# Kernel tuning notes

Hardware: AMD Instinct MI355X
Metric: run time of the kernel (lower is better)

Reference implementation:

```python
import jax, jax.numpy as jnp
import numpy as np

NUM_GROUPS = 32
EPS = 1e-5


def group_norm(x, w, b):
    # x: [B,C,H,W], 32 groups
    B, C, H, W = x.shape
    xg = x.reshape(B, NUM_GROUPS, C // NUM_GROUPS, H, W)
    mean = xg.mean(axis=(2, 3, 4), keepdims=True)
    var = xg.var(axis=(2, 3, 4), keepdims=True)
    xn = ((xg - mean) * jax.lax.rsqrt(var + EPS)).reshape(B, C, H, W)
    return xn * w[None, :, None, None] + b[None, :, None, None]


def conv1x1(x, w, b):
    # x: [B,C,H,W], w: [O,C], b: [O]
    return jnp.einsum('bchw,oc->bohw', x, w) + b[None, :, None, None]


def setup_inputs() -> dict:
    key = jax.random.key(0)
    ks = jax.random.split(key, 7)
    B, C, H, W = 16, 512, 32, 32
    x = jax.random.normal(ks[0], (B, C, H, W), dtype=jnp.float32)
    gn_w = jnp.ones((C,), dtype=jnp.float32)
    gn_b = jnp.zeros((C,), dtype=jnp.float32)
    s = 1.0 / np.sqrt(C)
    qkv_w = jax.random.normal(ks[1], (3 * C, C), dtype=jnp.float32) * s
    qkv_b = jnp.zeros((3 * C,), dtype=jnp.float32)
    proj_w = jax.random.normal(ks[2], (C, C), dtype=jnp.float32) * s
    proj_b = jnp.zeros((C,), dtype=jnp.float32)
    return {"x": x, "gn_w": gn_w, "gn_b": gn_b, "qkv_w": qkv_w,
            "qkv_b": qkv_b, "proj_w": proj_w, "proj_b": proj_b}


def reference(x, gn_w, gn_b, qkv_w, qkv_b, proj_w, proj_b):
    B, C, H, W = x.shape
    qkv = conv1x1(group_norm(x, gn_w, gn_b), qkv_w, qkv_b)
    q, k, v = jnp.split(qkv, 3, axis=1)
    scale = (C // 8) ** (-0.5)
    # attn: [B, h, w, H, W]
    attn = jnp.einsum('bchw,bcHW->bhwHW', q * scale, k)
    # NOTE: faithful to original torch code: softmax over the LAST axis only
    attn = jax.nn.softmax(attn, axis=-1)
    out = jnp.einsum('bhwHW,bcHW->bchw', attn, v)
    return x + conv1x1(out, proj_w, proj_b)
```

## Files before the change

kernel.cpp:

```cpp
#include <hip/hip_runtime.h>
#include <hip/hip_bf16.h>

#define B_    16
#define C_    512
#define S_    1024
#define NGRP  32
#define CPG   16

typedef __attribute__((ext_vector_type(8))) short  short8;
typedef __attribute__((ext_vector_type(4))) short  short4v;
typedef __attribute__((ext_vector_type(4))) float  floatx4;

__device__ __forceinline__ unsigned short f2bf(float f) {
    __hip_bfloat16 h = __float2bfloat16(f);
    unsigned short u;
    __builtin_memcpy(&u, &h, 2);
    return u;
}

__global__ __launch_bounds__(256)
void prep_kernel(const float* __restrict__ qkv_w, const float* __restrict__ proj_w,
                 const float* __restrict__ qkv_b,
                 unsigned short* __restrict__ bufX,
                 unsigned short* __restrict__ bufY,
                 float* __restrict__ bqWk, float* __restrict__ biasvp)
{
    int blk = blockIdx.x;
    int tid = threadIdx.x;
    if (blk < 192) {
        __shared__ float T[64][65];
        int mat = blk >> 6, tile = blk & 63;
        int r0 = (tile >> 3) * 64, c0 = (tile & 7) * 64;
        const float* src; unsigned short* dst;
        if (mat == 0)      { src = qkv_w + 512 * 512;  dst = bufX; }
        else if (mat == 1) { src = qkv_w;              dst = bufY; }
        else               { src = qkv_w + 1024 * 512; dst = bufY + 262144; }
#pragma unroll
        for (int rr = 0; rr < 4; ++rr) {
            int sr = rr * 16 + (tid >> 4);
            int sc = (tid & 15) * 4;
            float4 v = *(const float4*)(src + (size_t)(c0 + sr) * 512 + r0 + sc);
            T[sc][sr] = v.x; T[sc + 1][sr] = v.y; T[sc + 2][sr] = v.z; T[sc + 3][sr] = v.w;
        }
        __syncthreads();
#pragma unroll
        for (int rr = 0; rr < 4; ++rr) {
            int dr = rr * 16 + (tid >> 4);
            int dc = (tid & 15) * 4;
            short4v o;
            o[0] = (short)f2bf(T[dr][dc]);     o[1] = (short)f2bf(T[dr][dc + 1]);
            o[2] = (short)f2bf(T[dr][dc + 2]); o[3] = (short)f2bf(T[dr][dc + 3]);
            *(short4v*)(dst + (size_t)(r0 + dr) * 512 + c0 + dc) = o;
        }
    } else if (blk < 256) {
        unsigned short* wp = bufX + 262144;
#pragma unroll
        for (int t = 0; t < 4; ++t) {
            int i = (blk - 192) * 4096 + t * 1024 + tid * 4;
            float4 v = *(const float4*)(proj_w + i);
            short4v o;
            o[0] = (short)f2bf(v.x); o[1] = (short)f2bf(v.y);
            o[2] = (short)f2bf(v.z); o[3] = (short)f2bf(v.w);
            *(short4v*)(wp + i) = o;
        }
    } else if (blk < 264) {
        int sub = blk - 256;
        int j = (sub & 1) * 256 + tid;
        int o0 = (sub >> 1) * 128;
        float acc = 0.f;
#pragma unroll 8
        for (int oo = 0; oo < 128; ++oo) {
            int o = o0 + oo;
            acc += qkv_b[o] * qkv_w[(size_t)(512 + o) * 512 + j];
        }
        atomicAdd(&bqWk[j], acc);
    } else {
        int wv = tid >> 6, lane = tid & 63;
        int c = (blk - 264) * 4 + wv;
        float s = 0.f;
#pragma unroll
        for (int t = 0; t < 8; ++t)
            s += proj_w[(size_t)c * 512 + t * 64 + lane] * qkv_b[1024 + t * 64 + lane];
        for (int off = 32; off > 0; off >>= 1) s += __shfl_down(s, off);
        if (lane == 0) biasvp[c] = s;
    }
}

__global__ __launch_bounds__(256)
void gn_plus_w(const float* __restrict__ x, const float* __restrict__ gnw,
               const float* __restrict__ gnb, __hip_bfloat16* __restrict__ xnT,
               const unsigned short* __restrict__ bufX,
               const unsigned short* __restrict__ bufY,
               unsigned short* __restrict__ bufZ)
{
    __shared__ __align__(16) char smem[32832];
    int blk = blockIdx.x;
    int tid = threadIdx.x;

    if (blk < 512) {
        int b = blk >> 5, g = blk & 31;
        const float4* xp = (const float4*)(x + (size_t)blk * (CPG * S_));
        float4 vv[16];
        float s = 0.f, ss = 0.f;
#pragma unroll
        for (int r = 0; r < 16; ++r) {
            float4 v = xp[r * 256 + tid];
            vv[r] = v;
            s  += v.x + v.y + v.z + v.w;
            ss += v.x*v.x + v.y*v.y + v.z*v.z + v.w*v.w;
        }
        for (int off = 32; off > 0; off >>= 1) {
            s  += __shfl_down(s, off);
            ss += __shfl_down(ss, off);
        }
        float* red = (float*)(smem + 32768);
        float* msh = (float*)(smem + 32800);
        int wid = tid >> 6, lane = tid & 63;
        if (lane == 0) { red[wid] = s; red[4 + wid] = ss; }
        __syncthreads();
        if (tid == 0) {
            float a = 0.f, c = 0.f;
            for (int i = 0; i < 4; ++i) { a += red[i]; c += red[4 + i]; }
            float mean = a / (float)(CPG * S_);
            float var  = c / (float)(CPG * S_) - mean * mean;
            msh[0] = mean;
            msh[1] = rsqrtf(var + 1e-5f);
        }
        __syncthreads();
        float mean = msh[0], inv = msh[1];

        float sc[16], sh[16];
#pragma unroll
        for (int c = 0; c < 16; ++c) {
            float wc = gnw[g * 16 + c];
            sc[c] = inv * wc;
            sh[c] = gnb[g * 16 + c] - mean * inv * wc;
        }
#pragma unroll
        for (int kk = 0; kk < 4; ++kk) {
            unsigned short outp[16];
#pragma unroll
            for (int c = 0; c < 16; ++c) {
                float v = (kk == 0) ? vv[c].x : (kk == 1) ? vv[c].y : (kk == 2) ? vv[c].z : vv[c].w;
                outp[c] = f2bf(v * sc[c] + sh[c]);
            }
            int srow = 4 * tid + kk;
            unsigned short* dst = (unsigned short*)xnT + ((size_t)(b * S_ + srow) * C_ + g * 16);
            *(short8*)dst       = *(short8*)outp;
            *(short8*)(dst + 8) = *(short8*)(outp + 8);
        }
    } else {
        unsigned short* As = (unsigned short*)smem;
        unsigned short* Bs = (unsigned short*)(smem + 16384);
        int id = blk - 512;
        int bx = id & 3, by = (id >> 2) & 3, bz = id >> 4;
        const unsigned short* Ab = bufX + (size_t)bz * 262144;
        const unsigned short* Bb = bufY + (size_t)bz * 262144;
        __hip_bfloat16* Y = (__hip_bfloat16*)bufZ + (size_t)bz * 262144;
        const int wave = tid >> 6, lane = tid & 63;
        const int m0 = by * 128, n0 = bx * 128;
        const int wr = wave >> 1, wc = wave & 1, lr = lane & 15, kq = lane >> 4;
        const int row0 = tid >> 2, kc0 = (tid & 3) << 3;

        floatx4 acc[4][4] = {};
        for (int k0 = 0; k0 < 512; k0 += 64) {
            __syncthreads();
#pragma unroll
            for (int kk = 0; kk < 2; ++kk) {
#pragma unroll
                for (int r = 0; r < 2; ++r) {
                    const unsigned short* ga = Ab + (size_t)(m0 + r * 64 + row0) * 512 + k0 + kk * 32 + kc0;
                    __builtin_amdgcn_global_load_lds(
                        (const __attribute__((address_space(1))) void*)ga,
                        (__attribute__((address_space(3))) void*)(As + kk * 4096 + (r * 256 + wave * 64) * 8),
                        16, 0, 0);
                    const unsigned short* gb = Bb + (size_t)(n0 + r * 64 + row0) * 512 + k0 + kk * 32 + kc0;
                    __builtin_amdgcn_global_load_lds(
                        (const __attribute__((address_space(1))) void*)gb,
                        (__attribute__((address_space(3))) void*)(Bs + kk * 4096 + (r * 256 + wave * 64) * 8),
                        16, 0, 0);
                }
            }
            __syncthreads();
#pragma unroll
            for (int kk = 0; kk < 2; ++kk) {
                short8 af[4], bfr[4];
#pragma unroll
                for (int i = 0; i < 4; ++i)
                    af[i] = *(const short8*)&As[kk * 4096 + (wr * 64 + i * 16 + lr) * 32 + kq * 8];
#pragma unroll
                for (int j = 0; j < 4; ++j)
                    bfr[j] = *(const short8*)&Bs[kk * 4096 + (wc * 64 + j * 16 + lr) * 32 + kq * 8];
#pragma unroll
                for (int i = 0; i < 4; ++i)
#pragma unroll
                    for (int j = 0; j < 4; ++j)
                        acc[i][j] = __builtin_amdgcn_mfma_f32_16x16x32_bf16(af[i], bfr[j], acc[i][j], 0, 0, 0);
            }
        }
#pragma unroll
        for (int i = 0; i < 4; ++i)
#pragma unroll
            for (int r = 0; r < 4; ++r) {
                int m = m0 + wr * 64 + i * 16 + kq * 4 + r;
#pragma unroll
                for (int j = 0; j < 4; ++j) {
                    int n = n0 + wc * 64 + j * 16 + lr;
                    Y[(size_t)m * 512 + n] = __float2bfloat16(acc[i][j][r]);
                }
            }
    }
}

template<int BIAS_MODE>
__device__ __forceinline__
void gemm8_body(char* lds, const unsigned short* __restrict__ Ab,
                const unsigned short* __restrict__ Bb,
                const float* __restrict__ bias,
                __hip_bfloat16* __restrict__ Y,
                int lda, int ldb, int ldy, size_t ybase, int m0, int n0)
{
    char* asb = lds;
    char* bsb = lds + 32768;
    const int tid = threadIdx.x, wave = tid >> 6, lane = tid & 63;
    const int wr = wave >> 2, wc = wave & 3;
    const int lr = lane & 15, kq = lane >> 4;
    const int swz = (lr & 7) << 4;

    floatx4 acc[4][4] = {};
    short8 aF[2][2], bF[2][2][2];

    auto stage = [&](const unsigned short* __restrict__ G, int ld, int grow,
                     int t, char* dstbase) {
#pragma unroll
        for (int c = 0; c < 2; ++c) {
            int x = c * 8192 + tid * 16;
            int row = x >> 7;
            int colb = (x & 127) ^ ((row & 7) << 4);
            const unsigned short* ga = G + (size_t)(grow + row) * ld + t * 64 + (colb >> 1);
            char* ldst = dstbase + c * 8192 + wave * 1024;
            __builtin_amdgcn_global_load_lds(
                (const __attribute__((address_space(1))) void*)ga,
                (__attribute__((address_space(3))) void*)ldst, 16, 0, 0);
        }
    };
    auto rdA = [&](int buf, int i, int kk) {
        int byte = buf * 16384 + (wr * 64 + i * 16 + lr) * 128
                 + ((kk * 64 + kq * 16) ^ swz);
        return *(const short8*)(asb + byte);
    };
    auto rdB = [&](int buf, int jn, int kk) {
        int row = wc * 64 + jn * 16 + lr;
        int byte = buf * 32768 + (row >> 7) * 16384 + (row & 127) * 128
                 + ((kk * 64 + kq * 16) ^ swz);
        return *(const short8*)(bsb + byte);
    };

    stage(Ab, lda, m0,       0, asb);
    stage(Bb, ldb, n0,       0, bsb);
    stage(Bb, ldb, n0 + 128, 0, bsb + 16384);
    stage(Bb, ldb, n0,       1, bsb + 32768);
    stage(Bb, ldb, n0 + 128, 1, bsb + 32768 + 16384);
    asm volatile("s_waitcnt vmcnt(4)" ::: "memory");
    __builtin_amdgcn_s_barrier();

    constexpr int NT = 8;
    for (int t = 0; t < NT; ++t) {
        const int buf = t & 1;
#pragma unroll
        for (int ii = 0; ii < 2; ++ii) { aF[ii][0] = rdA(buf, ii, 0); aF[ii][1] = rdA(buf, ii, 1); }
#pragma unroll
        for (int jj = 0; jj < 2; ++jj) { bF[0][jj][0] = rdB(buf, jj, 0); bF[0][jj][1] = rdB(buf, jj, 1); }
        if (t < NT - 1) stage(Ab, lda, m0, t + 1, asb + ((t + 1) & 1) * 16384);
        __builtin_amdgcn_s_barrier();
        asm volatile("s_waitcnt lgkmcnt(0)" ::: "memory");
        __builtin_amdgcn_s_setprio(1);
#pragma unroll
        for (int ii = 0; ii < 2; ++ii)
#pragma unroll
            for (int jj = 0; jj < 2; ++jj)
#pragma unroll
                for (int kk = 0; kk < 2; ++kk)
                    acc[ii][jj] = __builtin_amdgcn_mfma_f32_16x16x32_bf16(aF[ii][kk], bF[0][jj][kk], acc[ii][jj], 0, 0, 0);
        __builtin_amdgcn_s_setprio(0);
        __builtin_amdgcn_s_barrier();
#pragma unroll
        for (int jj = 0; jj < 2; ++jj) { bF[1][jj][0] = rdB(buf, 2 + jj, 0); bF[1][jj][1] = rdB(buf, 2 + jj, 1); }
        __builtin_amdgcn_s_barrier();
        asm volatile("s_waitcnt lgkmcnt(0)" ::: "memory");
        __builtin_amdgcn_s_setprio(1);
#pragma unroll
        for (int ii = 0; ii < 2; ++ii)
#pragma unroll
            for (int jj = 0; jj < 2; ++jj)
#pragma unroll
                for (int kk = 0; kk < 2; ++kk)
                    acc[ii][2 + jj] = __builtin_amdgcn_mfma_f32_16x16x32_bf16(aF[ii][kk], bF[1][jj][kk], acc[ii][2 + jj], 0, 0, 0);
        __builtin_amdgcn_s_setprio(0);
        __builtin_amdgcn_s_barrier();
#pragma unroll
        for (int ii = 0; ii < 2; ++ii) { aF[ii][0] = rdA(buf, 2 + ii, 0); aF[ii][1] = rdA(buf, 2 + ii, 1); }
        if (t < NT - 2) stage(Bb, ldb, n0, t + 2, bsb + buf * 32768);
        __builtin_amdgcn_s_barrier();
        asm volatile("s_waitcnt lgkmcnt(0)" ::: "memory");
        __builtin_amdgcn_s_setprio(1);
#pragma unroll
        for (int ii = 0; ii < 2; ++ii)
#pragma unroll
            for (int jj = 0; jj < 2; ++jj)
#pragma unroll
                for (int kk = 0; kk < 2; ++kk)
                    acc[2 + ii][2 + jj] = __builtin_amdgcn_mfma_f32_16x16x32_bf16(aF[ii][kk], bF[1][jj][kk], acc[2 + ii][2 + jj], 0, 0, 0);
        __builtin_amdgcn_s_setprio(0);
        __builtin_amdgcn_s_barrier();
        if (t < NT - 2) stage(Bb, ldb, n0 + 128, t + 2, bsb + buf * 32768 + 16384);
        __builtin_amdgcn_s_setprio(1);
#pragma unroll
        for (int ii = 0; ii < 2; ++ii)
#pragma unroll
            for (int jj = 0; jj < 2; ++jj)
#pragma unroll
                for (int kk = 0; kk < 2; ++kk)
                    acc[2 + ii][jj] = __builtin_amdgcn_mfma_f32_16x16x32_bf16(aF[ii][kk], bF[0][jj][kk], acc[2 + ii][jj], 0, 0, 0);
        __builtin_amdgcn_s_setprio(0);
        if (t < NT - 2) { asm volatile("s_waitcnt vmcnt(4)" ::: "memory"); }
        else            { asm volatile("s_waitcnt vmcnt(0)" ::: "memory"); }
        __builtin_amdgcn_s_barrier();
    }

#pragma unroll
    for (int i = 0; i < 4; ++i)
#pragma unroll
        for (int r = 0; r < 4; ++r) {
            int m = m0 + wr * 64 + i * 16 + kq * 4 + r;
            float bm = (BIAS_MODE == 1) ? bias[m] : 0.f;
#pragma unroll
            for (int j = 0; j < 4; ++j) {
                int n = n0 + wc * 64 + j * 16 + lr;
                float vv = acc[i][j][r] + bm;
                if (BIAS_MODE == 2) vv += bias[n];
                Y[ybase + (size_t)m * ldy + n] = __float2bfloat16(vv);
            }
        }
}

__global__ __launch_bounds__(512)
void fused_s45(const unsigned short* __restrict__ xnT,
               const unsigned short* __restrict__ bufZ,
               const float* __restrict__ bqWk, const float* __restrict__ bvp,
               __hip_bfloat16* __restrict__ u, __hip_bfloat16* __restrict__ Vp)
{
    __shared__ __align__(16) char lds[98304];
    int blk = blockIdx.x;
    if (blk < 256) {
        int by = blk >> 1, bx = blk & 1;
        gemm8_body<2>(lds, xnT, bufZ, bqWk, u,
                      512, 512, 512, 0, by * 128, bx * 256);
    } else {
        int lin = blk - 256;
        int xcd = lin & 7, sup = lin >> 3;
        int bz = xcd + ((sup >> 4) << 3);
        int tile = sup & 15;
        int bx = tile & 3, by = tile >> 2;
        gemm8_body<1>(lds, bufZ + 262144, xnT + (size_t)bz * ((size_t)S_ * 512),
                      bvp, Vp,
                      512, 512, 1024, (size_t)bz * 512 * S_, by * 128, bx * 256);
    }
}

template<int BIAS_MODE, bool OUT_BF16, bool RESID, bool SWIZ, int KTOT>
__global__ __launch_bounds__(512)
void gemm8ph(const unsigned short* __restrict__ A, const unsigned short* __restrict__ Bm,
             const float* __restrict__ bias, const float* __restrict__ resid,
             void* __restrict__ Yv,
             int lda, int ldb, int ldy,
             size_t sA, size_t sB, size_t sY, size_t sR, float alpha,
             int ntsh, int nxsh)
{
    __shared__ __align__(16) char lds[98304];
    char* asb = lds;
    char* bsb = lds + 32768;

    int bx, by, bz;
    if (SWIZ) {
        int lin = blockIdx.x;
        int xcd = lin & 7, sup = lin >> 3;
        bz = xcd + ((sup >> ntsh) << 3);
        int tile = sup & ((1 << ntsh) - 1);
        bx = tile & ((1 << nxsh) - 1);
        by = tile >> nxsh;
    } else { bx = blockIdx.x; by = blockIdx.y; bz = blockIdx.z; }

    const unsigned short* Ab = A  + (size_t)bz * sA;
    const unsigned short* Bb = Bm + (size_t)bz * sB;
    const int tid = threadIdx.x, wave = tid >> 6, lane = tid & 63;
    const int m0 = by * 128, n0 = bx * 256;
    const int wr = wave >> 2, wc = wave & 3;
    const int lr = lane & 15, kq = lane >> 4;
    const int swz = (lr & 7) << 4;

    floatx4 acc[4][4] = {};
    short8 aF[2][2], bF[2][2][2];

    auto stage = [&](const unsigned short* __restrict__ G, int ld, int grow,
                     int t, char* dstbase) {
#pragma unroll
        for (int c = 0; c < 2; ++c) {
            int x = c * 8192 + tid * 16;
            int row = x >> 7;
            int colb = (x & 127) ^ ((row & 7) << 4);
            const unsigned short* ga = G + (size_t)(grow + row) * ld + t * 64 + (colb >> 1);
            char* ldst = dstbase + c * 8192 + wave * 1024;
            __builtin_amdgcn_global_load_lds(
                (const __attribute__((address_space(1))) void*)ga,
                (__attribute__((address_space(3))) void*)ldst, 16, 0, 0);
        }
    };
    auto rdA = [&](int buf, int i, int kk) {
        int byte = buf * 16384 + (wr * 64 + i * 16 + lr) * 128
                 + ((kk * 64 + kq * 16) ^ swz);
        return *(const short8*)(asb + byte);
    };
    auto rdB = [&](int buf, int jn, int kk) {
        int row = wc * 64 + jn * 16 + lr;
        int byte = buf * 32768 + (row >> 7) * 16384 + (row & 127) * 128
                 + ((kk * 64 + kq * 16) ^ swz);
        return *(const short8*)(bsb + byte);
    };

    stage(Ab, lda, m0,       0, asb);
    stage(Bb, ldb, n0,       0, bsb);
    stage(Bb, ldb, n0 + 128, 0, bsb + 16384);
    stage(Bb, ldb, n0,       1, bsb + 32768);
    stage(Bb, ldb, n0 + 128, 1, bsb + 32768 + 16384);
    asm volatile("s_waitcnt vmcnt(4)" ::: "memory");
    __builtin_amdgcn_s_barrier();

    constexpr int NT = KTOT / 64;
    for (int t = 0; t < NT; ++t) {
        const int buf = t & 1;
#pragma unroll
        for (int ii = 0; ii < 2; ++ii) { aF[ii][0] = rdA(buf, ii, 0); aF[ii][1] = rdA(buf, ii, 1); }
#pragma unroll
        for (int jj = 0; jj < 2; ++jj) { bF[0][jj][0] = rdB(buf, jj, 0); bF[0][jj][1] = rdB(buf, jj, 1); }
        if (t < NT - 1) stage(Ab, lda, m0, t + 1, asb + ((t + 1) & 1) * 16384);
        __builtin_amdgcn_s_barrier();
        asm volatile("s_waitcnt lgkmcnt(0)" ::: "memory");
        __builtin_amdgcn_s_setprio(1);
#pragma unroll
        for (int ii = 0; ii < 2; ++ii)
#pragma unroll
            for (int jj = 0; jj < 2; ++jj)
#pragma unroll
                for (int kk = 0; kk < 2; ++kk)
                    acc[ii][jj] = __builtin_amdgcn_mfma_f32_16x16x32_bf16(aF[ii][kk], bF[0][jj][kk], acc[ii][jj], 0, 0, 0);
        __builtin_amdgcn_s_setprio(0);
        __builtin_amdgcn_s_barrier();
#pragma unroll
        for (int jj = 0; jj < 2; ++jj) { bF[1][jj][0] = rdB(buf, 2 + jj, 0); bF[1][jj][1] = rdB(buf, 2 + jj, 1); }
        __builtin_amdgcn_s_barrier();
        asm volatile("s_waitcnt lgkmcnt(0)" ::: "memory");
        __builtin_amdgcn_s_setprio(1);
#pragma unroll
        for (int ii = 0; ii < 2; ++ii)
#pragma unroll
            for (int jj = 0; jj < 2; ++jj)
#pragma unroll
                for (int kk = 0; kk < 2; ++kk)
                    acc[ii][2 + jj] = __builtin_amdgcn_mfma_f32_16x16x32_bf16(aF[ii][kk], bF[1][jj][kk], acc[ii][2 + jj], 0, 0, 0);
        __builtin_amdgcn_s_setprio(0);
        __builtin_amdgcn_s_barrier();
#pragma unroll
        for (int ii = 0; ii < 2; ++ii) { aF[ii][0] = rdA(buf, 2 + ii, 0); aF[ii][1] = rdA(buf, 2 + ii, 1); }
        if (t < NT - 2) stage(Bb, ldb, n0, t + 2, bsb + buf * 32768);
        __builtin_amdgcn_s_barrier();
        asm volatile("s_waitcnt lgkmcnt(0)" ::: "memory");
        __builtin_amdgcn_s_setprio(1);
#pragma unroll
        for (int ii = 0; ii < 2; ++ii)
#pragma unroll
            for (int jj = 0; jj < 2; ++jj)
#pragma unroll
                for (int kk = 0; kk < 2; ++kk)
                    acc[2 + ii][2 + jj] = __builtin_amdgcn_mfma_f32_16x16x32_bf16(aF[ii][kk], bF[1][jj][kk], acc[2 + ii][2 + jj], 0, 0, 0);
        __builtin_amdgcn_s_setprio(0);
        __builtin_amdgcn_s_barrier();
        if (t < NT - 2) stage(Bb, ldb, n0 + 128, t + 2, bsb + buf * 32768 + 16384);
        __builtin_amdgcn_s_setprio(1);
#pragma unroll
        for (int ii = 0; ii < 2; ++ii)
#pragma unroll
            for (int jj = 0; jj < 2; ++jj)
#pragma unroll
                for (int kk = 0; kk < 2; ++kk)
                    acc[2 + ii][jj] = __builtin_amdgcn_mfma_f32_16x16x32_bf16(aF[ii][kk], bF[0][jj][kk], acc[2 + ii][jj], 0, 0, 0);
        __builtin_amdgcn_s_setprio(0);
        if (t < NT - 2) { asm volatile("s_waitcnt vmcnt(4)" ::: "memory"); }
        else            { asm volatile("s_waitcnt vmcnt(0)" ::: "memory"); }
        __builtin_amdgcn_s_barrier();
    }

    const size_t ybase = (size_t)bz * sY;
    const size_t rbase = (size_t)bz * sR;
#pragma unroll
    for (int i = 0; i < 4; ++i) {
#pragma unroll
        for (int r = 0; r < 4; ++r) {
            int m = m0 + wr * 64 + i * 16 + kq * 4 + r;
            float bm = (BIAS_MODE == 1) ? bias[m] : 0.f;
#pragma unroll
            for (int j = 0; j < 4; ++j) {
                int n = n0 + wc * 64 + j * 16 + lr;
                float vv = acc[i][j][r] * alpha + bm;
                if (BIAS_MODE == 2) vv += bias[n];
                if (RESID) vv += resid[rbase + (size_t)m * ldy + n];
                if (OUT_BF16)
                    ((__hip_bfloat16*)Yv)[ybase + (size_t)m * ldy + n] = __float2bfloat16(vv);
                else
                    ((float*)Yv)[ybase + (size_t)m * ldy + n] = vv;
            }
        }
    }
}

__global__ __launch_bounds__(512)
void scores_softmax8(const unsigned short* __restrict__ A,
                     const unsigned short* __restrict__ Bm,
                     unsigned short* __restrict__ P)
{
    __shared__ __align__(16) unsigned short lds[65536];
    char* asb = (char*)lds;
    char* bsb = (char*)lds + 65536;

    const int bid = blockIdx.x;
    const int bz = bid >> 4, t16 = bid & 15;
    const int by = t16 >> 2, bx = t16 & 3;
    const int m0 = by << 8, n0 = bx << 8;

    const size_t sAB = (size_t)S_ * 512;
    const unsigned short* Ab = A  + (size_t)bz * sAB;
    const unsigned short* Bb = Bm + (size_t)bz * sAB;

    const int tid = threadIdx.x, wave = tid >> 6, lane = tid & 63;
    const int wr = wave >> 2, wc = wave & 3;
    const int lr = lane & 15, kq = lane >> 4;
    const int swz = (lr & 7) << 4;

    floatx4 acc[8][4] = {};
    short8 aF[4][2], bF[2][2][2];

    auto stage = [&](const unsigned short* __restrict__ G, int row0, int t,
                     char* base, int buf, int half) {
#pragma unroll
        for (int c = 0; c < 2; ++c) {
            int x = c * 8192 + tid * 16;
            int row = x >> 7;
            int colb = (x & 127) ^ ((row & 7) << 4);
            const unsigned short* ga = G + (((size_t)(row0 + row)) << 9) + (t << 6) + (colb >> 1);
            char* ldst = base + buf * 32768 + half * 16384 + c * 8192 + wave * 1024;
            __builtin_amdgcn_global_load_lds(
                (const __attribute__((address_space(1))) void*)ga,
                (__attribute__((address_space(3))) void*)ldst, 16, 0, 0);
        }
    };
    auto rdA = [&](int buf, int mh, int ii, int kk) {
        int byte = buf * 32768 + wr * 16384 + (mh * 64 + ii * 16 + lr) * 128
                 + ((kk * 64 + kq * 16) ^ swz);
        return *(const short8*)(asb + byte);
    };
    auto rdB = [&](int buf, int nh, int jj, int kk) {
        int trow = wc * 64 + (nh * 2 + jj) * 16 + lr;
        int byte = buf * 32768 + (trow >> 7) * 16384 + (trow & 127) * 128
                 + ((kk * 64 + kq * 16) ^ swz);
        return *(const short8*)(bsb + byte);
    };

    stage(Ab, m0,       0, asb, 0, 0);
    stage(Bb, n0,       0, bsb, 0, 0);
    stage(Bb, n0 + 128, 0, bsb, 0, 1);
    stage(Ab, m0 + 128, 0, asb, 0, 1);
    stage(Ab, m0,       1, asb, 1, 0);
    stage(Bb, n0,       1, bsb, 1, 0);
    stage(Bb, n0 + 128, 1, bsb, 1, 1);
    asm volatile("s_waitcnt vmcnt(6)" ::: "memory");
    __builtin_amdgcn_s_barrier();

    for (int t = 0; t < 8; ++t) {
        const int buf = t & 1;
#pragma unroll
        for (int ii = 0; ii < 4; ++ii) { aF[ii][0] = rdA(buf, 0, ii, 0); aF[ii][1] = rdA(buf, 0, ii, 1); }
#pragma unroll
        for (int jj = 0; jj < 2; ++jj) { bF[0][jj][0] = rdB(buf, 0, jj, 0); bF[0][jj][1] = rdB(buf, 0, jj, 1); }
        if (t < 7) stage(Ab, m0 + 128, t + 1, asb, (t + 1) & 1, 1);
        __builtin_amdgcn_s_barrier();
        asm volatile("s_waitcnt lgkmcnt(0)" ::: "memory");
        __builtin_amdgcn_s_setprio(1);
#pragma unroll
        for (int ii = 0; ii < 4; ++ii)
#pragma unroll
            for (int jj = 0; jj < 2; ++jj)
#pragma unroll
                for (int kk = 0; kk < 2; ++kk)
                    acc[ii][jj] = __builtin_amdgcn_mfma_f32_16x16x32_bf16(aF[ii][kk], bF[0][jj][kk], acc[ii][jj], 0, 0, 0);
        __builtin_amdgcn_s_setprio(0);
        __builtin_amdgcn_s_barrier();
#pragma unroll
        for (int jj = 0; jj < 2; ++jj) { bF[1][jj][0] = rdB(buf, 1, jj, 0); bF[1][jj][1] = rdB(buf, 1, jj, 1); }
        __builtin_amdgcn_s_barrier();
        asm volatile("s_waitcnt lgkmcnt(0)" ::: "memory");
        __builtin_amdgcn_s_setprio(1);
#pragma unroll
        for (int ii = 0; ii < 4; ++ii)
#pragma unroll
            for (int jj = 0; jj < 2; ++jj)
#pragma unroll
                for (int kk = 0; kk < 2; ++kk)
                    acc[ii][2 + jj] = __builtin_amdgcn_mfma_f32_16x16x32_bf16(aF[ii][kk], bF[1][jj][kk], acc[ii][2 + jj], 0, 0, 0);
        __builtin_amdgcn_s_setprio(0);
        __builtin_amdgcn_s_barrier();
#pragma unroll
        for (int ii = 0; ii < 4; ++ii) { aF[ii][0] = rdA(buf, 1, ii, 0); aF[ii][1] = rdA(buf, 1, ii, 1); }
        if (t < 6) stage(Bb, n0, t + 2, bsb, buf, 0);
        __builtin_amdgcn_s_barrier();
        asm volatile("s_waitcnt lgkmcnt(0)" ::: "memory");
        __builtin_amdgcn_s_setprio(1);
#pragma unroll
        for (int ii = 0; ii < 4; ++ii)
#pragma unroll
            for (int jj = 0; jj < 2; ++jj)
#pragma unroll
                for (int kk = 0; kk < 2; ++kk)
                    acc[4 + ii][2 + jj] = __builtin_amdgcn_mfma_f32_16x16x32_bf16(aF[ii][kk], bF[1][jj][kk], acc[4 + ii][2 + jj], 0, 0, 0);
        __builtin_amdgcn_s_setprio(0);
        __builtin_amdgcn_s_barrier();
        if (t < 6) {
            stage(Ab, m0,       t + 2, asb, buf, 0);
            stage(Bb, n0 + 128, t + 2, bsb, buf, 1);
        }
        __builtin_amdgcn_s_setprio(1);
#pragma unroll
        for (int ii = 0; ii < 4; ++ii)
#pragma unroll
            for (int jj = 0; jj < 2; ++jj)
#pragma unroll
                for (int kk = 0; kk < 2; ++kk)
                    acc[4 + ii][jj] = __builtin_amdgcn_mfma_f32_16x16x32_bf16(aF[ii][kk], bF[0][jj][kk], acc[4 + ii][jj], 0, 0, 0);
        __builtin_amdgcn_s_setprio(0);
        if (t < 6) { asm volatile("s_waitcnt vmcnt(6)" ::: "memory"); }
        else       { asm volatile("s_waitcnt vmcnt(0)" ::: "memory"); }
        __builtin_amdgcn_s_barrier();
    }

#pragma unroll
    for (int j = 0; j < 4; ++j) {
        int sqc = wc * 64 + j * 16 + lr;
        int srow = sqc * 512;
        int sxor = (sqc & 7) << 4;
#pragma unroll
        for (int h = 0; h < 4; ++h) {
            float v0[4], v1[4];
            float mx = -1e30f;
#pragma unroll
            for (int r = 0; r < 4; ++r) {
                v0[r] = acc[2 * h][j][r]     * 0.125f;
                v1[r] = acc[2 * h + 1][j][r] * 0.125f;
                mx = fmaxf(mx, fmaxf(v0[r], v1[r]));
            }
            mx = fmaxf(mx, __shfl_xor(mx, 16));
            mx = fmaxf(mx, __shfl_xor(mx, 32));
            float sm = 0.f;
#pragma unroll
            for (int r = 0; r < 4; ++r) {
                v0[r] = __expf(v0[r] - mx);
                v1[r] = __expf(v1[r] - mx);
                sm += v0[r] + v1[r];
            }
            sm += __shfl_xor(sm, 16);
            sm += __shfl_xor(sm, 32);
            float inv = 1.f / sm;
            short4v p0, p1;
#pragma unroll
            for (int r = 0; r < 4; ++r) {
                p0[r] = (short)f2bf(v0[r] * inv);
                p1[r] = (short)f2bf(v1[r] * inv);
            }
            int kb = (wr * 128 + h * 32 + kq * 4) * 2;
            *(short4v*)(asb + ((srow + kb) ^ sxor))      = p0;
            *(short4v*)(asb + ((srow + kb + 32) ^ sxor)) = p1;
        }
    }
    __syncthreads();

    const size_t pbase = ((size_t)bz << 20) + (size_t)n0 * 1024 + m0;
#pragma unroll
    for (int it = 0; it < 16; ++it) {
        int row = wave * 32 + it * 2 + (lane >> 5);
        int colb = (lane & 31) << 4;
        short8 v = *(const short8*)(asb + ((row * 512 + colb) ^ ((row & 7) << 4)));
        *(short8*)(P + pbase + (size_t)row * 1024 + (colb >> 1)) = v;
    }
}

extern "C" void kernel_launch(void* const* d_in, const int* in_sizes, int n_in,
                              void* d_out, int out_size, void* d_ws, size_t ws_size,
                              hipStream_t stream) {
    const float* x     = (const float*)d_in[0];
    const float* gn_w  = (const float*)d_in[1];
    const float* gn_b  = (const float*)d_in[2];
    const float* qkv_w = (const float*)d_in[3];
    const float* qkv_b = (const float*)d_in[4];
    const float* pr_w  = (const float*)d_in[5];
    const float* pr_b  = (const float*)d_in[6];
    float* out = (float*)d_out;

    char* w = (char*)d_ws;
    __hip_bfloat16* xnT  = (__hip_bfloat16*)w;
    __hip_bfloat16* u    = (__hip_bfloat16*)(w + (16u << 20));
    __hip_bfloat16* Vp   = (__hip_bfloat16*)(w + (32u << 20));
    __hip_bfloat16* P    = (__hip_bfloat16*)(w + (48u << 20));
    unsigned short* bufX = (unsigned short*)(w + (80u << 20));
    unsigned short* bufY = (unsigned short*)(w + (81u << 20));
    unsigned short* bufZ = (unsigned short*)(w + (82u << 20));
    float*          bqWk = (float*)(w + (83u << 20));
    float*          bvp  = (float*)(w + (83u << 20) + 4096);

    hipMemsetAsync(bqWk, 0, 512 * sizeof(float), stream);

    prep_kernel<<<392, 256, 0, stream>>>(qkv_w, pr_w, qkv_b, bufX, bufY, bqWk, bvp);

    gn_plus_w<<<544, 256, 0, stream>>>(x, gn_w, gn_b, xnT, bufX, bufY, bufZ);

    fused_s45<<<512, 512, 0, stream>>>((const unsigned short*)xnT, bufZ, bqWk, bvp,
                                       u, Vp);

    scores_softmax8<<<256, 512, 0, stream>>>(
        (const unsigned short*)xnT, (const unsigned short*)u, (unsigned short*)P);

    gemm8ph<1, false, true, true, 1024><<<256, 512, 0, stream>>>(
        (const unsigned short*)Vp, (const unsigned short*)P, pr_b, x, out,
        1024, 1024, 1024, (size_t)512 * S_, (size_t)S_ * S_, (size_t)512 * S_,
        (size_t)512 * S_, 1.f, 4, 2);
}
```

Before: 196.4 us.

## Enlarge fused GEMM tiles to 256x256 and halve the block count

The fused u/Vp GEMM body now computes 256x256 output tiles per 512-thread block instead of 128x256, doubling the A tile and the per-wave accumulators (8x4 fragments). Block count drops from 512 to 256, with LDS growing to 128 KB and a reworked stage/prefetch schedule. The goal is higher arithmetic intensity and less redundant B-operand traffic, at the cost of more registers, more LDS per block and only one wave of blocks across the CUs.

```diff
diff --git a/kernel.cpp b/kernel.cpp
--- a/kernel.cpp
+++ b/kernel.cpp
@@ -214,69 +214,71 @@
 
 template<int BIAS_MODE>
 __device__ __forceinline__
-void gemm8_body(char* lds, const unsigned short* __restrict__ Ab,
-                const unsigned short* __restrict__ Bb,
-                const float* __restrict__ bias,
-                __hip_bfloat16* __restrict__ Y,
-                int lda, int ldb, int ldy, size_t ybase, int m0, int n0)
+void gemm256_body(char* lds, const unsigned short* __restrict__ Ab,
+                  const unsigned short* __restrict__ Bb,
+                  const float* __restrict__ bias,
+                  __hip_bfloat16* __restrict__ Y,
+                  int ldy, size_t ybase, int m0, int n0)
 {
     char* asb = lds;
-    char* bsb = lds + 32768;
+    char* bsb = lds + 65536;
+
     const int tid = threadIdx.x, wave = tid >> 6, lane = tid & 63;
     const int wr = wave >> 2, wc = wave & 3;
     const int lr = lane & 15, kq = lane >> 4;
     const int swz = (lr & 7) << 4;
 
-    floatx4 acc[4][4] = {};
-    short8 aF[2][2], bF[2][2][2];
-
-    auto stage = [&](const unsigned short* __restrict__ G, int ld, int grow,
-                     int t, char* dstbase) {
+    floatx4 acc[8][4] = {};
+    short8 aF[4][2], bF[2][2][2];
+
+    auto stage = [&](const unsigned short* __restrict__ G, int row0, int t,
+                     char* base, int buf, int half) {
 #pragma unroll
         for (int c = 0; c < 2; ++c) {
             int x = c * 8192 + tid * 16;
             int row = x >> 7;
             int colb = (x & 127) ^ ((row & 7) << 4);
-            const unsigned short* ga = G + (size_t)(grow + row) * ld + t * 64 + (colb >> 1);
-            char* ldst = dstbase + c * 8192 + wave * 1024;
+            const unsigned short* ga = G + (((size_t)(row0 + row)) << 9) + (t << 6) + (colb >> 1);
+            char* ldst = base + buf * 32768 + half * 16384 + c * 8192 + wave * 1024;
             __builtin_amdgcn_global_load_lds(
                 (const __attribute__((address_space(1))) void*)ga,
                 (__attribute__((address_space(3))) void*)ldst, 16, 0, 0);
         }
     };
-    auto rdA = [&](int buf, int i, int kk) {
-        int byte = buf * 16384 + (wr * 64 + i * 16 + lr) * 128
+    auto rdA = [&](int buf, int mh, int ii, int kk) {
+        int byte = buf * 32768 + wr * 16384 + (mh * 64 + ii * 16 + lr) * 128
                  + ((kk * 64 + kq * 16) ^ swz);
         return *(const short8*)(asb + byte);
     };
-    auto rdB = [&](int buf, int jn, int kk) {
-        int row = wc * 64 + jn * 16 + lr;
-        int byte = buf * 32768 + (row >> 7) * 16384 + (row & 127) * 128
+    auto rdB = [&](int buf, int nh, int jj, int kk) {
+        int trow = wc * 64 + (nh * 2 + jj) * 16 + lr;
+        int byte = buf * 32768 + (trow >> 7) * 16384 + (trow & 127) * 128
                  + ((kk * 64 + kq * 16) ^ swz);
         return *(const short8*)(bsb + byte);
     };
 
-    stage(Ab, lda, m0,       0, asb);
-    stage(Bb, ldb, n0,       0, bsb);
-    stage(Bb, ldb, n0 + 128, 0, bsb + 16384);
-    stage(Bb, ldb, n0,       1, bsb + 32768);
-    stage(Bb, ldb, n0 + 128, 1, bsb + 32768 + 16384);
-    asm volatile("s_waitcnt vmcnt(4)" ::: "memory");
+    stage(Ab, m0,       0, asb, 0, 0);
+    stage(Bb, n0,       0, bsb, 0, 0);
+    stage(Bb, n0 + 128, 0, bsb, 0, 1);
+    stage(Ab, m0 + 128, 0, asb, 0, 1);
+    stage(Ab, m0,       1, asb, 1, 0);
+    stage(Bb, n0,       1, bsb, 1, 0);
+    stage(Bb, n0 + 128, 1, bsb, 1, 1);
+    asm volatile("s_waitcnt vmcnt(6)" ::: "memory");
     __builtin_amdgcn_s_barrier();
 
-    constexpr int NT = 8;
-    for (int t = 0; t < NT; ++t) {
+    for (int t = 0; t < 8; ++t) {
         const int buf = t & 1;
 #pragma unroll
-        for (int ii = 0; ii < 2; ++ii) { aF[ii][0] = rdA(buf, ii, 0); aF[ii][1] = rdA(buf, ii, 1); }
-#pragma unroll
-        for (int jj = 0; jj < 2; ++jj) { bF[0][jj][0] = rdB(buf, jj, 0); bF[0][jj][1] = rdB(buf, jj, 1); }
-        if (t < NT - 1) stage(Ab, lda, m0, t + 1, asb + ((t + 1) & 1) * 16384);
-        __builtin_amdgcn_s_barrier();
-        asm volatile("s_waitcnt lgkmcnt(0)" ::: "memory");
-        __builtin_amdgcn_s_setprio(1);
-#pragma unroll
-        for (int ii = 0; ii < 2; ++ii)
+        for (int ii = 0; ii < 4; ++ii) { aF[ii][0] = rdA(buf, 0, ii, 0); aF[ii][1] = rdA(buf, 0, ii, 1); }
+#pragma unroll
+        for (int jj = 0; jj < 2; ++jj) { bF[0][jj][0] = rdB(buf, 0, jj, 0); bF[0][jj][1] = rdB(buf, 0, jj, 1); }
+        if (t < 7) stage(Ab, m0 + 128, t + 1, asb, (t + 1) & 1, 1);
+        __builtin_amdgcn_s_barrier();
+        asm volatile("s_waitcnt lgkmcnt(0)" ::: "memory");
+        __builtin_amdgcn_s_setprio(1);
+#pragma unroll
+        for (int ii = 0; ii < 4; ++ii)
 #pragma unroll
             for (int jj = 0; jj < 2; ++jj)
 #pragma unroll
@@ -285,12 +287,12 @@
         __builtin_amdgcn_s_setprio(0);
         __builtin_amdgcn_s_barrier();
 #pragma unroll
-        for (int jj = 0; jj < 2; ++jj) { bF[1][jj][0] = rdB(buf, 2 + jj, 0); bF[1][jj][1] = rdB(buf, 2 + jj, 1); }
-        __builtin_amdgcn_s_barrier();
-        asm volatile("s_waitcnt lgkmcnt(0)" ::: "memory");
-        __builtin_amdgcn_s_setprio(1);
-#pragma unroll
-        for (int ii = 0; ii < 2; ++ii)
+        for (int jj = 0; jj < 2; ++jj) { bF[1][jj][0] = rdB(buf, 1, jj, 0); bF[1][jj][1] = rdB(buf, 1, jj, 1); }
+        __builtin_amdgcn_s_barrier();
+        asm volatile("s_waitcnt lgkmcnt(0)" ::: "memory");
+        __builtin_amdgcn_s_setprio(1);
+#pragma unroll
+        for (int ii = 0; ii < 4; ++ii)
 #pragma unroll
             for (int jj = 0; jj < 2; ++jj)
 #pragma unroll
@@ -299,45 +301,48 @@
         __builtin_amdgcn_s_setprio(0);
         __builtin_amdgcn_s_barrier();
 #pragma unroll
-        for (int ii = 0; ii < 2; ++ii) { aF[ii][0] = rdA(buf, 2 + ii, 0); aF[ii][1] = rdA(buf, 2 + ii, 1); }
-        if (t < NT - 2) stage(Bb, ldb, n0, t + 2, bsb + buf * 32768);
-        __builtin_amdgcn_s_barrier();
-        asm volatile("s_waitcnt lgkmcnt(0)" ::: "memory");
-        __builtin_amdgcn_s_setprio(1);
-#pragma unroll
-        for (int ii = 0; ii < 2; ++ii)
-#pragma unroll
-            for (int jj = 0; jj < 2; ++jj)
-#pragma unroll
-                for (int kk = 0; kk < 2; ++kk)
-                    acc[2 + ii][2 + jj] = __builtin_amdgcn_mfma_f32_16x16x32_bf16(aF[ii][kk], bF[1][jj][kk], acc[2 + ii][2 + jj], 0, 0, 0);
-        __builtin_amdgcn_s_setprio(0);
-        __builtin_amdgcn_s_barrier();
-        if (t < NT - 2) stage(Bb, ldb, n0 + 128, t + 2, bsb + buf * 32768 + 16384);
-        __builtin_amdgcn_s_setprio(1);
-#pragma unroll
-        for (int ii = 0; ii < 2; ++ii)
-#pragma unroll
-            for (int jj = 0; jj < 2; ++jj)
-#pragma unroll
-                for (int kk = 0; kk < 2; ++kk)
-                    acc[2 + ii][jj] = __builtin_amdgcn_mfma_f32_16x16x32_bf16(aF[ii][kk], bF[0][jj][kk], acc[2 + ii][jj], 0, 0, 0);
-        __builtin_amdgcn_s_setprio(0);
-        if (t < NT - 2) { asm volatile("s_waitcnt vmcnt(4)" ::: "memory"); }
-        else            { asm volatile("s_waitcnt vmcnt(0)" ::: "memory"); }
-        __builtin_amdgcn_s_barrier();
-    }
-
-#pragma unroll
-    for (int i = 0; i < 4; ++i)
+        for (int ii = 0; ii < 4; ++ii) { aF[ii][0] = rdA(buf, 1, ii, 0); aF[ii][1] = rdA(buf, 1, ii, 1); }
+        if (t < 6) stage(Bb, n0, t + 2, bsb, buf, 0);
+        __builtin_amdgcn_s_barrier();
+        asm volatile("s_waitcnt lgkmcnt(0)" ::: "memory");
+        __builtin_amdgcn_s_setprio(1);
+#pragma unroll
+        for (int ii = 0; ii < 4; ++ii)
+#pragma unroll
+            for (int jj = 0; jj < 2; ++jj)
+#pragma unroll
+                for (int kk = 0; kk < 2; ++kk)
+                    acc[4 + ii][2 + jj] = __builtin_amdgcn_mfma_f32_16x16x32_bf16(aF[ii][kk], bF[1][jj][kk], acc[4 + ii][2 + jj], 0, 0, 0);
+        __builtin_amdgcn_s_setprio(0);
+        __builtin_amdgcn_s_barrier();
+        if (t < 6) {
+            stage(Ab, m0,       t + 2, asb, buf, 0);
+            stage(Bb, n0 + 128, t + 2, bsb, buf, 1);
+        }
+        __builtin_amdgcn_s_setprio(1);
+#pragma unroll
+        for (int ii = 0; ii < 4; ++ii)
+#pragma unroll
+            for (int jj = 0; jj < 2; ++jj)
+#pragma unroll
+                for (int kk = 0; kk < 2; ++kk)
+                    acc[4 + ii][jj] = __builtin_amdgcn_mfma_f32_16x16x32_bf16(aF[ii][kk], bF[0][jj][kk], acc[4 + ii][jj], 0, 0, 0);
+        __builtin_amdgcn_s_setprio(0);
+        if (t < 6) { asm volatile("s_waitcnt vmcnt(6)" ::: "memory"); }
+        else       { asm volatile("s_waitcnt vmcnt(0)" ::: "memory"); }
+        __builtin_amdgcn_s_barrier();
+    }
+
+#pragma unroll
+    for (int idx = 0; idx < 8; ++idx)
 #pragma unroll
         for (int r = 0; r < 4; ++r) {
-            int m = m0 + wr * 64 + i * 16 + kq * 4 + r;
+            int m = m0 + wr * 128 + idx * 16 + kq * 4 + r;
             float bm = (BIAS_MODE == 1) ? bias[m] : 0.f;
 #pragma unroll
             for (int j = 0; j < 4; ++j) {
                 int n = n0 + wc * 64 + j * 16 + lr;
-                float vv = acc[i][j][r] + bm;
+                float vv = acc[idx][j][r] + bm;
                 if (BIAS_MODE == 2) vv += bias[n];
                 Y[ybase + (size_t)m * ldy + n] = __float2bfloat16(vv);
             }
@@ -350,21 +355,19 @@
                const float* __restrict__ bqWk, const float* __restrict__ bvp,
                __hip_bfloat16* __restrict__ u, __hip_bfloat16* __restrict__ Vp)
 {
-    __shared__ __align__(16) char lds[98304];
+    __shared__ __align__(16) char lds[131072];
     int blk = blockIdx.x;
-    if (blk < 256) {
+    if (blk < 128) {
         int by = blk >> 1, bx = blk & 1;
-        gemm8_body<2>(lds, xnT, bufZ, bqWk, u,
-                      512, 512, 512, 0, by * 128, bx * 256);
+        gemm256_body<2>(lds, xnT, bufZ, bqWk, u, 512, 0, by * 256, bx * 256);
     } else {
-        int lin = blk - 256;
+        int lin = blk - 128;
         int xcd = lin & 7, sup = lin >> 3;
-        int bz = xcd + ((sup >> 4) << 3);
-        int tile = sup & 15;
+        int bz = xcd + ((sup >> 3) << 3);
+        int tile = sup & 7;
         int bx = tile & 3, by = tile >> 2;
-        gemm8_body<1>(lds, bufZ + 262144, xnT + (size_t)bz * ((size_t)S_ * 512),
-                      bvp, Vp,
-                      512, 512, 1024, (size_t)bz * 512 * S_, by * 128, bx * 256);
+        gemm256_body<1>(lds, bufZ + 262144, xnT + (size_t)bz * ((size_t)S_ * 512),
+                        bvp, Vp, 1024, (size_t)bz * 512 * S_, by * 256, bx * 256);
     }
 }
 
@@ -730,7 +733,7 @@
 
     gn_plus_w<<<544, 256, 0, stream>>>(x, gn_w, gn_b, xnT, bufX, bufY, bufZ);
 
-    fused_s45<<<512, 512, 0, stream>>>((const unsigned short*)xnT, bufZ, bqWk, bvp,
+    fused_s45<<<256, 512, 0, stream>>>((const unsigned short*)xnT, bufZ, bqWk, bvp,
                                        u, Vp);
 
     scores_softmax8<<<256, 512, 0, stream>>>(
```

Result: faster. 190.0 us, median of 2 (-3.3%).
